# Optimization experiments

Measured on AMD Instinct MI355X. Metric: run time of the kernel, lower is better.

Reference implementation:

```python
import jax, jax.numpy as jnp
import numpy as np

N_NODES = 100000
N_EDGES = 1250000
D_FEAT = 64


def setup_inputs() -> dict:
    key = jax.random.key(0)
    kx, ke = jax.random.split(key)
    x = jax.random.normal(kx, (N_NODES, D_FEAT), dtype=jnp.float32)
    edge_index = jax.random.randint(ke, (2, N_EDGES), 0, N_NODES, dtype=jnp.int64)
    return {"x": x, "edge_index": edge_index}


def reference(x, edge_index):
    # adj[src, dst] = 1; x_neighbors = adj.T @ x  ->
    # x_neighbors[i] = sum_{edges (s, d) with d == i} x[s]
    src, dst = edge_index[0], edge_index[1]
    msgs = x[src]  # [n_edges, d_feat] gather
    x_neighbors = jax.ops.segment_sum(msgs, dst, num_segments=x.shape[0])
    return x_neighbors
```

## Files before the change

### kernel.cpp

```cpp
#include <hip/hip_runtime.h>
#include <hip/hip_bf16.h>

#define N_NODES 100000
#define N_EDGES 1250000
#define D_FEAT  64
#define SB_NODES 512
#define SB_SHIFT 9
#define NSB     196
#define CAP_SB  7040
#define OVF_CAP 8192
#define EPB_I4  1024
#define N_I4    (N_EDGES / 4)
#define NBLK_BUILD ((N_I4 + EPB_I4 - 1) / EPB_I4)
#define RT      512

__global__ __launch_bounds__(256) void to_bf16(
    const float* __restrict__ x, ushort* __restrict__ xh, uint* __restrict__ fill)
{
    if (blockIdx.x == 0) {
        for (int i = threadIdx.x; i < NSB + 2; i += 256) fill[i] = 0u;
    }
    int t = blockIdx.x * 256 + threadIdx.x;
    const float4* x4 = (const float4*)x;
    float4 a = x4[2 * t];
    float4 b = x4[2 * t + 1];
    float f[8] = {a.x, a.y, a.z, a.w, b.x, b.y, b.z, b.w};
    uint h[8];
#pragma unroll
    for (int i = 0; i < 8; ++i) {
        uint u = __float_as_uint(f[i]);
        u += 0x7FFFu + ((u >> 16) & 1u);
        h[i] = u >> 16;
    }
    uint4 o;
    o.x = h[0] | (h[1] << 16);
    o.y = h[2] | (h[3] << 16);
    o.z = h[4] | (h[5] << 16);
    o.w = h[6] | (h[7] << 16);
    ((uint4*)xh)[t] = o;
}

__global__ __launch_bounds__(256) void build_sb(
    const int* __restrict__ src, const int* __restrict__ dst,
    uint* __restrict__ fill, uint* __restrict__ pairs,
    uint* __restrict__ ovfCnt, int2* __restrict__ ovf)
{
    __shared__ uint cnt[NSB];
    __shared__ uint base[NSB];
    const int t = threadIdx.x;
    for (int i = t; i < NSB; i += 256) cnt[i] = 0;
    __syncthreads();

    uint   pw[16];
    ushort pb[16];
    ushort pr[16];
    bool   vk[4];
    const int i40 = blockIdx.x * EPB_I4;
#pragma unroll
    for (int k = 0; k < 4; ++k) {
        int i4 = i40 + t + k * 256;
        vk[k] = (i4 < N_I4);
        if (vk[k]) {
            int4 d4 = ((const int4*)dst)[i4];
            int4 s4 = ((const int4*)src)[i4];
            int dd[4] = {d4.x, d4.y, d4.z, d4.w};
            int ss[4] = {s4.x, s4.y, s4.z, s4.w};
#pragma unroll
            for (int j = 0; j < 4; ++j) {
                uint b = ((uint)dd[j]) >> SB_SHIFT;
                uint r = atomicAdd(&cnt[b], 1u);
                pw[k * 4 + j] = ((((uint)dd[j]) & (SB_NODES - 1u)) << 17) | (uint)ss[j];
                pb[k * 4 + j] = (ushort)b;
                pr[k * 4 + j] = (ushort)r;
            }
        }
    }
    __syncthreads();

    for (int i = t; i < NSB; i += 256) {
        uint c = cnt[i];
        base[i] = c ? atomicAdd(&fill[i], c) : 0u;
    }
    __syncthreads();

#pragma unroll
    for (int j = 0; j < 16; ++j) {
        if (vk[j >> 2]) {
            uint b = pb[j];
            uint g = base[b] + pr[j];
            if (g < CAP_SB) {
                pairs[(size_t)b * CAP_SB + g] = pw[j];
            } else {
                uint o = atomicAdd(ovfCnt, 1u);
                if (o < OVF_CAP)
                    ovf[o] = make_int2((int)(pw[j] & 0x1FFFFu),
                                       (int)((b << SB_SHIFT) | (pw[j] >> 17)));
            }
        }
    }
}

__global__ __launch_bounds__(RT) void repart(
    uint* __restrict__ pairs, const uint* __restrict__ fill,
    uint* __restrict__ offs)
{
    __shared__ uint pw[CAP_SB];
    __shared__ int  cnt[SB_NODES];
    __shared__ int  scn[SB_NODES];
    __shared__ int  pos[SB_NODES];

    const int t  = threadIdx.x;
    const int sb = blockIdx.x;
    const int n  = min((int)fill[sb], CAP_SB);
    const size_t base = (size_t)sb * CAP_SB;

    cnt[t] = 0;
    __syncthreads();
    for (int i = t; i < n; i += RT) {
        uint w = pairs[base + i];
        pw[i] = w;
        atomicAdd(&cnt[w >> 17], 1);
    }
    __syncthreads();

    scn[t] = cnt[t];
    __syncthreads();
    for (int off = 1; off < SB_NODES; off <<= 1) {
        int v = (t >= off) ? scn[t - off] : 0;
        __syncthreads();
        scn[t] += v;
        __syncthreads();
    }
    {
        int e = scn[t] - cnt[t];
        pos[t] = e;
        offs[sb * SB_NODES + t] = (uint)e | ((uint)cnt[t] << 16);
    }
    __syncthreads();

    for (int i = t; i < n; i += RT) {
        uint w = pw[i];
        int r = atomicAdd(&pos[w >> 17], 1);
        pairs[base + r] = w & 0x1FFFFu;
    }
}

__global__ __launch_bounds__(256) void gather_csr(
    const ushort* __restrict__ xh, const uint* __restrict__ pairs,
    const uint* __restrict__ offs, const float* __restrict__ x,
    const int2* __restrict__ ovf, const uint* __restrict__ ovfCnt,
    float* __restrict__ out)
{
    const int t    = threadIdx.x;
    const int lane = t & 63;
    const int sub  = lane >> 3;
    const int l8   = lane & 7;
    const int node = blockIdx.x * 4 + (t >> 6);
    if (node >= N_NODES) return;
    const uint4* __restrict__ xrow = (const uint4*)xh;

    const uint v    = offs[node];
    const int start = (node >> SB_SHIFT) * CAP_SB + (int)(v & 0xFFFFu);
    const int deg   = (int)(v >> 16);

    float f[8];
#pragma unroll
    for (int j = 0; j < 8; ++j) f[j] = 0.f;

    int i = sub;
    for (; i + 8 < deg; i += 16) {
        uint s0 = pairs[start + i];
        uint s1 = pairs[start + i + 8];
        uint4 v0 = xrow[(size_t)s0 * 8 + l8];
        uint4 v1 = xrow[(size_t)s1 * 8 + l8];
        f[0] += __uint_as_float((v0.x & 0xFFFFu) << 16);
        f[1] += __uint_as_float(v0.x & 0xFFFF0000u);
        f[2] += __uint_as_float((v0.y & 0xFFFFu) << 16);
        f[3] += __uint_as_float(v0.y & 0xFFFF0000u);
        f[4] += __uint_as_float((v0.z & 0xFFFFu) << 16);
        f[5] += __uint_as_float(v0.z & 0xFFFF0000u);
        f[6] += __uint_as_float((v0.w & 0xFFFFu) << 16);
        f[7] += __uint_as_float(v0.w & 0xFFFF0000u);
        f[0] += __uint_as_float((v1.x & 0xFFFFu) << 16);
        f[1] += __uint_as_float(v1.x & 0xFFFF0000u);
        f[2] += __uint_as_float((v1.y & 0xFFFFu) << 16);
        f[3] += __uint_as_float(v1.y & 0xFFFF0000u);
        f[4] += __uint_as_float((v1.z & 0xFFFFu) << 16);
        f[5] += __uint_as_float(v1.z & 0xFFFF0000u);
        f[6] += __uint_as_float((v1.w & 0xFFFFu) << 16);
        f[7] += __uint_as_float(v1.w & 0xFFFF0000u);
    }
    if (i < deg) {
        uint s0 = pairs[start + i];
        uint4 v0 = xrow[(size_t)s0 * 8 + l8];
        f[0] += __uint_as_float((v0.x & 0xFFFFu) << 16);
        f[1] += __uint_as_float(v0.x & 0xFFFF0000u);
        f[2] += __uint_as_float((v0.y & 0xFFFFu) << 16);
        f[3] += __uint_as_float(v0.y & 0xFFFF0000u);
        f[4] += __uint_as_float((v0.z & 0xFFFFu) << 16);
        f[5] += __uint_as_float(v0.z & 0xFFFF0000u);
        f[6] += __uint_as_float((v0.w & 0xFFFFu) << 16);
        f[7] += __uint_as_float(v0.w & 0xFFFF0000u);
    }

#pragma unroll
    for (int j = 0; j < 8; ++j) {
        f[j] += __shfl_xor(f[j], 8, 64);
        f[j] += __shfl_xor(f[j], 16, 64);
        f[j] += __shfl_xor(f[j], 32, 64);
    }

    const int nov = min((int)*ovfCnt, OVF_CAP);
    for (int e = 0; e < nov; ++e) {
        int2 p = ovf[e];
        if (p.y == node) {
            float4 a = ((const float4*)x)[(size_t)p.x * 16 + l8 * 2];
            float4 b = ((const float4*)x)[(size_t)p.x * 16 + l8 * 2 + 1];
            f[0] += a.x; f[1] += a.y; f[2] += a.z; f[3] += a.w;
            f[4] += b.x; f[5] += b.y; f[6] += b.z; f[7] += b.w;
        }
    }

    if (lane < 8) {
        float4* out4 = (float4*)out;
        out4[(size_t)node * 16 + l8 * 2]     = make_float4(f[0], f[1], f[2], f[3]);
        out4[(size_t)node * 16 + l8 * 2 + 1] = make_float4(f[4], f[5], f[6], f[7]);
    }
}

extern "C" void kernel_launch(void* const* d_in, const int* in_sizes, int n_in,
                              void* d_out, int out_size, void* d_ws, size_t ws_size,
                              hipStream_t stream) {
    const float* x = (const float*)d_in[0];
    const int* edge_index = (const int*)d_in[1];
    const int* src = edge_index;
    const int* dst = edge_index + N_EDGES;
    float* out = (float*)d_out;

    ushort* xh     = (ushort*)d_ws;
    uint*   pairs  = (uint*)(xh + (size_t)N_NODES * D_FEAT);
    uint*   offs   = pairs + (size_t)NSB * CAP_SB;
    uint*   fill   = offs + NSB * SB_NODES;
    uint*   ovfCnt = fill + NSB;
    int2*   ovf    = (int2*)(fill + NSB + 2);

    to_bf16<<<(N_NODES * D_FEAT / 8) / 256, 256, 0, stream>>>(x, xh, fill);
    build_sb<<<NBLK_BUILD, 256, 0, stream>>>(src, dst, fill, pairs, ovfCnt, ovf);
    repart<<<NSB, RT, 0, stream>>>(pairs, fill, offs);
    gather_csr<<<(N_NODES + 3) / 4, 256, 0, stream>>>(xh, pairs, offs, x, ovf, ovfCnt, out);
}
```

Before: 142.7 us.

## Stage bucketed edges in shared memory for coalesced scatter writes

In build_sb, edges are first sorted locally by super-bucket through a block-wide prefix scan into shared staging arrays. They are then written out in bucket-contiguous order, so consecutive threads write adjacent addresses in pairs. In repart, the sorted edges are placed in a shared buffer and copied back linearly, replacing random global writes. The cost is an extra block-level scan with many barriers, more shared memory in build_sb (about 24KB), and a second global read of pairs in repart.

```diff
diff --git a/kernel.cpp b/kernel.cpp
--- a/kernel.cpp
+++ b/kernel.cpp
@@ -45,10 +45,14 @@
     uint* __restrict__ fill, uint* __restrict__ pairs,
     uint* __restrict__ ovfCnt, int2* __restrict__ ovf)
 {
-    __shared__ uint cnt[NSB];
-    __shared__ uint base[NSB];
+    __shared__ uint cnt[256];
+    __shared__ uint scn[256];
+    __shared__ uint sbase[NSB];
+    __shared__ uint   stw[EPB_I4 * 4];
+    __shared__ ushort stb[EPB_I4 * 4];
+
     const int t = threadIdx.x;
-    for (int i = t; i < NSB; i += 256) cnt[i] = 0;
+    cnt[t] = 0;
     __syncthreads();
 
     uint   pw[16];
@@ -77,25 +81,45 @@
     }
     __syncthreads();
 
-    for (int i = t; i < NSB; i += 256) {
-        uint c = cnt[i];
-        base[i] = c ? atomicAdd(&fill[i], c) : 0u;
-    }
-    __syncthreads();
+    if (t < NSB) {
+        uint c = cnt[t];
+        sbase[t] = c ? atomicAdd(&fill[t], c) : 0u;
+    }
+
+    scn[t] = cnt[t];
+    __syncthreads();
+#pragma unroll
+    for (int off = 1; off < 256; off <<= 1) {
+        uint v = (t >= off) ? scn[t - off] : 0u;
+        __syncthreads();
+        scn[t] += v;
+        __syncthreads();
+    }
 
 #pragma unroll
     for (int j = 0; j < 16; ++j) {
         if (vk[j >> 2]) {
             uint b = pb[j];
-            uint g = base[b] + pr[j];
-            if (g < CAP_SB) {
-                pairs[(size_t)b * CAP_SB + g] = pw[j];
-            } else {
-                uint o = atomicAdd(ovfCnt, 1u);
-                if (o < OVF_CAP)
-                    ovf[o] = make_int2((int)(pw[j] & 0x1FFFFu),
-                                       (int)((b << SB_SHIFT) | (pw[j] >> 17)));
-            }
+            uint p = scn[b] - cnt[b] + pr[j];
+            stw[p] = pw[j];
+            stb[p] = (ushort)b;
+        }
+    }
+    __syncthreads();
+
+    const int m = (int)scn[255];
+    for (int j = t; j < m; j += 256) {
+        uint w = stw[j];
+        uint b = stb[j];
+        uint local = (uint)j - (scn[b] - cnt[b]);
+        uint g = sbase[b] + local;
+        if (g < CAP_SB) {
+            pairs[(size_t)b * CAP_SB + g] = w;
+        } else {
+            uint o = atomicAdd(ovfCnt, 1u);
+            if (o < OVF_CAP)
+                ovf[o] = make_int2((int)(w & 0x1FFFFu),
+                                   (int)((b << SB_SHIFT) | (w >> 17)));
         }
     }
 }
@@ -104,7 +128,7 @@
     uint* __restrict__ pairs, const uint* __restrict__ fill,
     uint* __restrict__ offs)
 {
-    __shared__ uint pw[CAP_SB];
+    __shared__ uint srt[CAP_SB];
     __shared__ int  cnt[SB_NODES];
     __shared__ int  scn[SB_NODES];
     __shared__ int  pos[SB_NODES];
@@ -118,7 +142,6 @@
     __syncthreads();
     for (int i = t; i < n; i += RT) {
         uint w = pairs[base + i];
-        pw[i] = w;
         atomicAdd(&cnt[w >> 17], 1);
     }
     __syncthreads();
@@ -139,10 +162,14 @@
     __syncthreads();
 
     for (int i = t; i < n; i += RT) {
-        uint w = pw[i];
+        uint w = pairs[base + i];
         int r = atomicAdd(&pos[w >> 17], 1);
-        pairs[base + r] = w & 0x1FFFFu;
-    }
+        srt[r] = w & 0x1FFFFu;
+    }
+    __syncthreads();
+
+    for (int i = t; i < n; i += RT)
+        pairs[base + i] = srt[i];
 }
 
 __global__ __launch_bounds__(256) void gather_csr(
```

Result: faster. 138.0 us (-3.3%).
